# Optimization experiments

Hardware: AMD Instinct MI355X
Metric: run time of the kernel (lower is better)

## Reference

```python
import jax, jax.numpy as jnp
import numpy as np
import math

N_HEADS = 16
D_EMB = 1024
D_HEAD = D_EMB // N_HEADS


def setup_inputs() -> dict:
    key = jax.random.key(0)
    ks = jax.random.split(key, 5)
    scale_in = 1.0 / math.sqrt(D_EMB)
    x = jax.random.normal(ks[0], (2, 2048, D_EMB), dtype=jnp.float32)
    w_in = jax.random.uniform(ks[1], (3 * D_EMB, D_EMB), dtype=jnp.float32, minval=-scale_in, maxval=scale_in)
    b_in = jax.random.uniform(ks[2], (3 * D_EMB,), dtype=jnp.float32, minval=-scale_in, maxval=scale_in)
    w_out = jax.random.uniform(ks[3], (D_EMB, D_EMB), dtype=jnp.float32, minval=-scale_in, maxval=scale_in)
    b_out = jax.random.uniform(ks[4], (D_EMB,), dtype=jnp.float32, minval=-scale_in, maxval=scale_in)
    return {"x": x, "w_in": w_in, "b_in": b_in, "w_out": w_out, "b_out": b_out, "apply_mask": 1}


def reference(x, w_in, b_in, w_out, b_out, apply_mask):
    B, S, D = x.shape
    # fused QKV projection: torch Linear uses y = x @ W^T + b
    qkv = jnp.einsum('bsd,ed->bse', x, w_in) + b_in  # [B,S,3D]
    q, k, v = jnp.split(qkv, 3, axis=-1)
    # [B,H,S,Dh]
    q = q.reshape(B, S, N_HEADS, D_HEAD).transpose(0, 2, 1, 3)
    k = k.reshape(B, S, N_HEADS, D_HEAD).transpose(0, 2, 1, 3)
    v = v.reshape(B, S, N_HEADS, D_HEAD).transpose(0, 2, 1, 3)
    w = jnp.einsum('bhqd,bhkd->bhqk', q, k)  # [B,H,S,S]
    if apply_mask:
        causal = jnp.triu(jnp.ones((S, S), dtype=bool), k=1)
        w = jnp.where(causal, -jnp.inf, w)
    w = w / jnp.sqrt(jnp.float32(D_HEAD)).astype(w.dtype)
    w = jax.nn.softmax(w, axis=-1)
    score = jnp.einsum('bhqk,bhkd->bhqd', w, v)  # [B,H,S,Dh]
    score = score.transpose(0, 2, 1, 3).reshape(B, S, D)
    return jnp.einsum('bsd,ed->bse', score, w_out) + b_out
```

## Files before the change

### kernel.cpp

```cpp
#include <hip/hip_runtime.h>
#include <stdint.h>

#define DEMB 1024
#define NHEAD 16
#define DHEAD 64
#define SEQ 2048
#define MROWS 4096

typedef __bf16 bf16x8 __attribute__((ext_vector_type(8)));
typedef float f32x4 __attribute__((ext_vector_type(4)));
typedef unsigned short u16;

#define LOG2E 1.44269504088896340736f

__device__ __forceinline__ u16 f2b(float f) {
  return __builtin_bit_cast(u16, (__bf16)f);
}
__device__ __forceinline__ uint32_t pk2(float a, float b) {
  return (uint32_t)f2b(a) | ((uint32_t)f2b(b) << 16);
}

__device__ __forceinline__ f32x4 mfma16(bf16x8 a, bf16x8 b, f32x4 c) {
  return __builtin_amdgcn_mfma_f32_16x16x32_bf16(a, b, c, 0, 0, 0);
}

__device__ __forceinline__ void gload_lds16(const void* g, void* l) {
  __builtin_amdgcn_global_load_lds(
      (__attribute__((address_space(1))) unsigned int*)(g),
      (__attribute__((address_space(3))) unsigned int*)(l), 16, 0, 0);
}

__global__ void cvt3_f32_bf16(const float* __restrict__ a, int na,
                              const float* __restrict__ b, int nb,
                              const float* __restrict__ c, int nc,
                              u16* __restrict__ da, u16* __restrict__ db,
                              u16* __restrict__ dc) {
  const int total = (na + nb + nc) >> 2;
  const int stride = gridDim.x * blockDim.x;
  for (int t = blockIdx.x * blockDim.x + threadIdx.x; t < total; t += stride) {
    int i = t << 2;
    const float* s;
    u16* d;
    if (i < na) {
      s = a + i; d = da + i;
    } else if (i < na + nb) {
      s = b + (i - na); d = db + (i - na);
    } else {
      s = c + (i - na - nb); d = dc + (i - na - nb);
    }
    float4 f = *(const float4*)s;
    ushort4 o;
    o.x = f2b(f.x); o.y = f2b(f.y); o.z = f2b(f.z); o.w = f2b(f.w);
    *(ushort4*)d = o;
  }
}

template <int EPI>
__global__ __launch_bounds__(256, 4) void gemm_nt(
    const u16* __restrict__ A, const u16* __restrict__ Bw,
    const float* __restrict__ bias, int K, int N,
    u16* __restrict__ q_out, u16* __restrict__ k_out, u16* __restrict__ v_out,
    float* __restrict__ f_out) {
  __shared__ __align__(16) u16 As[128 * 64];
  __shared__ __align__(16) u16 Bs[128 * 64];
  const int tid = threadIdx.x;
  const int w = tid >> 6;
  const int lane = tid & 63;
  const int wm = w >> 1, wn = w & 1;
  const int m0 = blockIdx.y * 128, n0 = blockIdx.x * 128;
  const int l16 = lane & 15, lg = lane >> 4;
  const int st_row = lane >> 3, st_slot = lane & 7;

  f32x4 acc[4][4] = {};

  for (int k0 = 0; k0 < K; k0 += 64) {
#pragma unroll
    for (int i = 0; i < 4; ++i) {
      const int chunk = (w << 2) | i;
      const int row = (chunk << 3) | st_row;
      const int scol = (st_slot ^ (row & 7)) << 3;
      gload_lds16(A + (size_t)(m0 + row) * K + k0 + scol, (char*)As + (chunk << 10));
      gload_lds16(Bw + (size_t)(n0 + row) * K + k0 + scol, (char*)Bs + (chunk << 10));
    }
    __syncthreads();
#pragma unroll
    for (int ks = 0; ks < 2; ++ks) {
      bf16x8 af[4], bfr[4];
#pragma unroll
      for (int mi = 0; mi < 4; ++mi) {
        const int row = wm * 64 + mi * 16 + l16;
        const int cb = ((ks << 6) | (lg << 4)) ^ ((row & 7) << 4);
        af[mi] = *(const bf16x8*)((const char*)As + row * 128 + cb);
      }
#pragma unroll
      for (int ni = 0; ni < 4; ++ni) {
        const int row = wn * 64 + ni * 16 + l16;
        const int cb = ((ks << 6) | (lg << 4)) ^ ((row & 7) << 4);
        bfr[ni] = *(const bf16x8*)((const char*)Bs + row * 128 + cb);
      }
#pragma unroll
      for (int mi = 0; mi < 4; ++mi)
#pragma unroll
        for (int ni = 0; ni < 4; ++ni)
          acc[mi][ni] = mfma16(af[mi], bfr[ni], acc[mi][ni]);
    }
    __syncthreads();
  }

#pragma unroll
  for (int ni = 0; ni < 4; ++ni) {
    const int n = n0 + wn * 64 + ni * 16 + l16;
    const float bv = bias[n];
    if (EPI == 0) {
      const int part = n >> 10;
      const int hh = (n >> 6) & 15;
      const int dh = n & 63;
      if (part == 2) {
#pragma unroll
        for (int mi = 0; mi < 4; ++mi) {
          const int mbase = m0 + wm * 64 + mi * 16 + (lg << 2);
          const int bq = mbase >> 11, s0 = mbase & 2047;
          ushort4 o;
          o.x = f2b(acc[mi][ni][0] + bv);
          o.y = f2b(acc[mi][ni][1] + bv);
          o.z = f2b(acc[mi][ni][2] + bv);
          o.w = f2b(acc[mi][ni][3] + bv);
          *(ushort4*)(v_out + ((size_t)(((bq << 4) | hh) * 64 + dh)) * SEQ + s0) = o;
        }
      } else {
        const float scl = (part == 0) ? (0.125f * LOG2E) : 1.0f;
        u16* dst = (part == 0) ? q_out : k_out;
#pragma unroll
        for (int mi = 0; mi < 4; ++mi) {
#pragma unroll
          for (int i = 0; i < 4; ++i) {
            const int m = m0 + wm * 64 + mi * 16 + (lg << 2) + i;
            const int bq = m >> 11, s = m & 2047;
            dst[((size_t)((bq << 4) | hh) * SEQ + s) * DHEAD + dh] = f2b((acc[mi][ni][i] + bv) * scl);
          }
        }
      }
    } else {
#pragma unroll
      for (int mi = 0; mi < 4; ++mi)
#pragma unroll
        for (int i = 0; i < 4; ++i) {
          const int m = m0 + wm * 64 + mi * 16 + (lg << 2) + i;
          f_out[(size_t)m * N + n] = acc[mi][ni][i] + bv;
        }
    }
  }
}

__device__ __forceinline__ int swz4(int r) { return (r ^ (r >> 3)) & 15; }

__device__ __forceinline__ void stage_k(const u16* __restrict__ Kb, size_t base,
                                        int jt, u16* Ks, int w, int lane) {
#pragma unroll
  for (int i = 0; i < 4; ++i) {
    const int g = (w << 2) | i;
    const int row = (g << 2) | (lane >> 4);
    const int shat = (lane & 15) ^ swz4(row);
    const int kv = (row << 1) | (shat >> 3);
    const int del = (shat & 7) << 3;
    gload_lds16(Kb + base + (size_t)(jt * 128 + kv) * DHEAD + del,
                (char*)Ks + (g << 10));
  }
}

__device__ __forceinline__ void stage_v(const u16* __restrict__ VTg, size_t base,
                                        int jt, u16* Vs, int w, int lane) {
#pragma unroll
  for (int i = 0; i < 4; ++i) {
    const int g = (w << 2) | i;
    const int row = (g << 2) | (lane >> 4);
    const int shat = (lane & 15) ^ swz4(row);
    gload_lds16(VTg + base + (size_t)row * SEQ + jt * 128 + (shat << 3),
                (char*)Vs + (g << 10));
  }
}

__global__ __launch_bounds__(256, 2) void attn_fwd(
    const u16* __restrict__ Qb, const u16* __restrict__ Kb,
    const u16* __restrict__ VTg, u16* __restrict__ Ob,
    const int* __restrict__ amask) {
  __shared__ __align__(16) u16 Ks[2][64 * 128];
  __shared__ __align__(16) u16 Vt[2][64 * 128];
  __shared__ __align__(16) uint32_t Ps[4][1024];
  const int tid = threadIdx.x;
  const int w = tid >> 6, lane = tid & 63;
  const int l16 = lane & 15, lg = lane >> 4;

  const int id = blockIdx.x;
  const int xcd = id & 7;
  const int r = id >> 3;
  const int bh = (xcd << 2) | (r & 3);
  const int p = r >> 2;
  const int qiA = 31 - p, qiB = p;

  const size_t base = (size_t)bh * (SEQ * DHEAD);
  const bool causal = (amask[0] != 0);
  const int ntA = causal ? ((qiA >> 1) + 1) : (SEQ / 128);
  const int ntB = causal ? ((qiB >> 1) + 1) : (SEQ / 128);
  const int nt = ntA + ntB;
  const int b = bh >> 4, h = bh & 15;

  int qseg0 = qiA * 64;

  bf16x8 qf[2];
  {
    const u16* qp = Qb + base + (size_t)(qseg0 + (w << 4) + l16) * DHEAD + (lg << 3);
    qf[0] = *(const bf16x8*)qp;
    qf[1] = *(const bf16x8*)(qp + 32);
  }

  float mrow = -1e30f, lrowp = 0.f;
  f32x4 oacc[4] = {};

  const int key = (l16 & 7) << 2;
  char* prow = (char*)(&Ps[w][0]) + l16 * 256;

  stage_k(Kb, base, 0, Ks[0], w, lane);
  stage_v(VTg, base, 0, Vt[0], w, lane);
  __syncthreads();

  int cur = 0;
  for (int t = 0; t < nt; ++t) {
    const int j = (t >= ntA) ? (t - ntA) : t;
    const u16* Kcur = Ks[cur];
    const u16* Vcur = Vt[cur];
    const bool pre = (t + 1 < nt);
    const int jn = (t + 1 >= ntA) ? (t + 1 - ntA) : (t + 1);
    if (pre) stage_k(Kb, base, jn, Ks[cur ^ 1], w, lane);

    f32x4 sv[8];
    __builtin_amdgcn_s_setprio(1);
#pragma unroll
    for (int nf = 0; nf < 8; ++nf) {
      const int row2 = (nf << 3) | (l16 >> 1);
      const int sz = swz4(row2);
      const int s0 = ((l16 & 1) << 3) | lg;
      bf16x8 kf0 = *(const bf16x8*)((const char*)Kcur + row2 * 256 + ((s0 ^ sz) << 4));
      bf16x8 kf1 = *(const bf16x8*)((const char*)Kcur + row2 * 256 + (((s0 | 4) ^ sz) << 4));
      f32x4 s = {};
      s = mfma16(kf0, qf[0], s);
      s = mfma16(kf1, qf[1], s);
      sv[nf] = s;
    }
    __builtin_amdgcn_s_setprio(0);

    const bool segEnd = (t == ntA - 1) || (t == nt - 1);
    if (causal && segEnd) {
      const int q = qseg0 + (w << 4) + l16;
#pragma unroll
      for (int nf = 0; nf < 8; ++nf)
#pragma unroll
        for (int i = 0; i < 4; ++i) {
          const int kv = j * 128 + (nf << 4) + (lg << 2) + i;
          if (kv > q) sv[nf][i] = -1e30f;
        }
    }

    float tmaxg;
    {
      f32x4 mt;
#pragma unroll
      for (int i = 0; i < 4; ++i) {
        const float a01 = fmaxf(sv[0][i], sv[1][i]);
        const float a23 = fmaxf(sv[2][i], sv[3][i]);
        const float a45 = fmaxf(sv[4][i], sv[5][i]);
        const float a67 = fmaxf(sv[6][i], sv[7][i]);
        mt[i] = fmaxf(fmaxf(a01, a23), fmaxf(a45, a67));
      }
      tmaxg = fmaxf(fmaxf(mt[0], mt[1]), fmaxf(mt[2], mt[3]));
      tmaxg = fmaxf(tmaxg, __shfl_xor(tmaxg, 16));
      tmaxg = fmaxf(tmaxg, __shfl_xor(tmaxg, 32));
    }

    if (__any(tmaxg > mrow + 8.0f)) {
      const float mnew = fmaxf(mrow, tmaxg);
      const float corr = __builtin_amdgcn_exp2f(mrow - mnew);
      lrowp *= corr;
#pragma unroll
      for (int df = 0; df < 4; ++df)
#pragma unroll
        for (int i = 0; i < 4; ++i) oacc[df][i] *= corr;
      mrow = mnew;
    }

#pragma unroll
    for (int nf = 0; nf < 8; ++nf) {
      const float p0 = __builtin_amdgcn_exp2f(sv[nf][0] - mrow);
      const float p1 = __builtin_amdgcn_exp2f(sv[nf][1] - mrow);
      const float p2 = __builtin_amdgcn_exp2f(sv[nf][2] - mrow);
      const float p3 = __builtin_amdgcn_exp2f(sv[nf][3] - mrow);
      lrowp += (p0 + p1) + (p2 + p3);
      uint2 pkv;
      pkv.x = pk2(p0, p1);
      pkv.y = pk2(p2, p3);
      const int word = ((nf << 3) | (lg << 1)) ^ key;
      *(uint2*)(prow + word * 4) = pkv;
    }

    if (pre) stage_v(VTg, base, jn, Vt[cur ^ 1], w, lane);

    bf16x8 pa[4];
#pragma unroll
    for (int s = 0; s < 4; ++s)
      pa[s] = *(const bf16x8*)(prow + ((((s << 4) | (lg << 2)) ^ key) << 2));

    __builtin_amdgcn_s_setprio(1);
#pragma unroll
    for (int df = 0; df < 4; ++df) {
      const int row = (df << 4) + l16;
      const int sz = swz4(row) << 4;
#pragma unroll
      for (int s = 0; s < 4; ++s) {
        bf16x8 vf = *(const bf16x8*)((const char*)Vcur + row * 256 + (((s << 6) | (lg << 4)) ^ sz));
        oacc[df] = mfma16(vf, pa[s], oacc[df]);
      }
    }
    __builtin_amdgcn_s_setprio(0);

    if (segEnd) {
      float lrow = lrowp + __shfl_xor(lrowp, 16);
      lrow += __shfl_xor(lrow, 32);
      const float inv = 1.0f / lrow;
      const int s = qseg0 + (w << 4) + l16;
      u16* orow = Ob + (size_t)(b * SEQ + s) * DEMB + h * DHEAD;
#pragma unroll
      for (int df = 0; df < 4; ++df) {
        ushort4 o;
        o.x = f2b(oacc[df][0] * inv);
        o.y = f2b(oacc[df][1] * inv);
        o.z = f2b(oacc[df][2] * inv);
        o.w = f2b(oacc[df][3] * inv);
        *(ushort4*)(orow + (df << 4) + (lg << 2)) = o;
      }
      if (t != nt - 1) {
        qseg0 = qiB * 64;
        mrow = -1e30f;
        lrowp = 0.f;
#pragma unroll
        for (int df = 0; df < 4; ++df)
#pragma unroll
          for (int i = 0; i < 4; ++i) oacc[df][i] = 0.f;
        const u16* qp = Qb + base + (size_t)(qseg0 + (w << 4) + l16) * DHEAD + (lg << 3);
        qf[0] = *(const bf16x8*)qp;
        qf[1] = *(const bf16x8*)(qp + 32);
      }
    }

    if (pre) __syncthreads();
    cur ^= 1;
  }
}

extern "C" void kernel_launch(void* const* d_in, const int* in_sizes, int n_in,
                              void* d_out, int out_size, void* d_ws, size_t ws_size,
                              hipStream_t stream) {
  const float* x = (const float*)d_in[0];
  const float* w_in = (const float*)d_in[1];
  const float* b_in = (const float*)d_in[2];
  const float* w_out = (const float*)d_in[3];
  const float* b_out = (const float*)d_in[4];
  const int* amask = (const int*)d_in[5];
  float* out = (float*)d_out;

  u16* xb = (u16*)d_ws;
  u16* wib = xb + (size_t)MROWS * DEMB;
  u16* wob = wib + (size_t)3 * DEMB * DEMB;
  u16* Qb = wob + (size_t)DEMB * DEMB;
  u16* Kb = Qb + (size_t)MROWS * DEMB;
  u16* Vtg = Kb + (size_t)MROWS * DEMB;
  u16* Ab = xb;

  cvt3_f32_bf16<<<2048, 256, 0, stream>>>(x, MROWS * DEMB, w_in, 3 * DEMB * DEMB,
                                          w_out, DEMB * DEMB, xb, wib, wob);

  gemm_nt<0><<<dim3(24, 32), 256, 0, stream>>>(xb, wib, b_in, DEMB, 3 * DEMB,
                                               Qb, Kb, Vtg, nullptr);
  attn_fwd<<<512, 256, 0, stream>>>(Qb, Kb, Vtg, Ab, amask);
  gemm_nt<1><<<dim3(8, 32), 256, 0, stream>>>(Ab, wob, b_out, DEMB, DEMB,
                                              nullptr, nullptr, nullptr, out);
}
```

Measured before the change: 102.8 us.

## Split attention into one query tile per block with 64-key tiles

The attention kernel previously paired two causal query tiles (long and short) per block with 128-key tiles. Now each block handles one 64-row query tile over 64-key tiles, with a grid of 1024 blocks ordered so heavy and light tiles interleave. LDS buffers are halved and launch bounds raised to 4 blocks per CU to increase occupancy. In exchange there are more loop iterations with more barriers per unit of work, less work per barrier, and load balance now depends on the block scheduling order.

```diff
diff --git a/kernel.cpp b/kernel.cpp
--- a/kernel.cpp
+++ b/kernel.cpp
@@ -154,62 +154,59 @@
 
 __device__ __forceinline__ int swz4(int r) { return (r ^ (r >> 3)) & 15; }
 
-__device__ __forceinline__ void stage_k(const u16* __restrict__ Kb, size_t base,
-                                        int jt, u16* Ks, int w, int lane) {
-#pragma unroll
-  for (int i = 0; i < 4; ++i) {
-    const int g = (w << 2) | i;
+__device__ __forceinline__ void stage_k64(const u16* __restrict__ Kb, size_t base,
+                                          int jt, u16* Ks, int w, int lane) {
+#pragma unroll
+  for (int i = 0; i < 2; ++i) {
+    const int g = (w << 1) | i;
     const int row = (g << 2) | (lane >> 4);
-    const int shat = (lane & 15) ^ swz4(row);
-    const int kv = (row << 1) | (shat >> 3);
-    const int del = (shat & 7) << 3;
-    gload_lds16(Kb + base + (size_t)(jt * 128 + kv) * DHEAD + del,
+    const int sh = (lane & 15) ^ swz4(row);
+    const int kv = (row << 1) | (sh >> 3);
+    const int del = (sh & 7) << 3;
+    gload_lds16(Kb + base + (size_t)(jt * 64 + kv) * DHEAD + del,
                 (char*)Ks + (g << 10));
   }
 }
 
-__device__ __forceinline__ void stage_v(const u16* __restrict__ VTg, size_t base,
-                                        int jt, u16* Vs, int w, int lane) {
-#pragma unroll
-  for (int i = 0; i < 4; ++i) {
-    const int g = (w << 2) | i;
+__device__ __forceinline__ void stage_v64(const u16* __restrict__ VTg, size_t base,
+                                          int jt, u16* Vs, int w, int lane) {
+#pragma unroll
+  for (int i = 0; i < 2; ++i) {
+    const int g = (w << 1) | i;
     const int row = (g << 2) | (lane >> 4);
-    const int shat = (lane & 15) ^ swz4(row);
-    gload_lds16(VTg + base + (size_t)row * SEQ + jt * 128 + (shat << 3),
+    const int sh = (lane & 15) ^ swz4(row);
+    const int d = (row << 1) | (sh >> 3);
+    gload_lds16(VTg + base + (size_t)d * SEQ + jt * 64 + ((sh & 7) << 3),
                 (char*)Vs + (g << 10));
   }
 }
 
-__global__ __launch_bounds__(256, 2) void attn_fwd(
+__global__ __launch_bounds__(256, 4) void attn_fwd(
     const u16* __restrict__ Qb, const u16* __restrict__ Kb,
     const u16* __restrict__ VTg, u16* __restrict__ Ob,
     const int* __restrict__ amask) {
-  __shared__ __align__(16) u16 Ks[2][64 * 128];
-  __shared__ __align__(16) u16 Vt[2][64 * 128];
-  __shared__ __align__(16) uint32_t Ps[4][1024];
+  __shared__ __align__(16) u16 Ks[2][32 * 128];
+  __shared__ __align__(16) u16 Vt[2][32 * 128];
+  __shared__ __align__(16) uint32_t Ps[4][512];
   const int tid = threadIdx.x;
   const int w = tid >> 6, lane = tid & 63;
   const int l16 = lane & 15, lg = lane >> 4;
 
   const int id = blockIdx.x;
-  const int xcd = id & 7;
-  const int r = id >> 3;
-  const int bh = (xcd << 2) | (r & 3);
-  const int p = r >> 2;
-  const int qiA = 31 - p, qiB = p;
+  const int k5 = id >> 5;
+  const int jj = k5 & 7, qq = k5 >> 3;
+  const int qi = (qq == 0) ? 31 - jj : (qq == 1) ? jj : (qq == 2) ? 23 - jj : 8 + jj;
+  const int bh = ((id & 7) << 2) | ((id >> 3) & 3);
 
   const size_t base = (size_t)bh * (SEQ * DHEAD);
   const bool causal = (amask[0] != 0);
-  const int ntA = causal ? ((qiA >> 1) + 1) : (SEQ / 128);
-  const int ntB = causal ? ((qiB >> 1) + 1) : (SEQ / 128);
-  const int nt = ntA + ntB;
+  const int nt = causal ? (qi + 1) : (SEQ / 64);
   const int b = bh >> 4, h = bh & 15;
-
-  int qseg0 = qiA * 64;
+  const int qrow = qi * 64 + (w << 4) + l16;
 
   bf16x8 qf[2];
   {
-    const u16* qp = Qb + base + (size_t)(qseg0 + (w << 4) + l16) * DHEAD + (lg << 3);
+    const u16* qp = Qb + base + (size_t)qrow * DHEAD + (lg << 3);
     qf[0] = *(const bf16x8*)qp;
     qf[1] = *(const bf16x8*)(qp + 32);
   }
@@ -218,30 +215,28 @@
   f32x4 oacc[4] = {};
 
   const int key = (l16 & 7) << 2;
-  char* prow = (char*)(&Ps[w][0]) + l16 * 256;
-
-  stage_k(Kb, base, 0, Ks[0], w, lane);
-  stage_v(VTg, base, 0, Vt[0], w, lane);
+  char* prow = (char*)(&Ps[w][0]) + l16 * 128;
+
+  stage_k64(Kb, base, 0, Ks[0], w, lane);
+  stage_v64(VTg, base, 0, Vt[0], w, lane);
   __syncthreads();
 
   int cur = 0;
   for (int t = 0; t < nt; ++t) {
-    const int j = (t >= ntA) ? (t - ntA) : t;
     const u16* Kcur = Ks[cur];
     const u16* Vcur = Vt[cur];
     const bool pre = (t + 1 < nt);
-    const int jn = (t + 1 >= ntA) ? (t + 1 - ntA) : (t + 1);
-    if (pre) stage_k(Kb, base, jn, Ks[cur ^ 1], w, lane);
-
-    f32x4 sv[8];
+    if (pre) stage_k64(Kb, base, t + 1, Ks[cur ^ 1], w, lane);
+
+    f32x4 sv[4];
     __builtin_amdgcn_s_setprio(1);
 #pragma unroll
-    for (int nf = 0; nf < 8; ++nf) {
-      const int row2 = (nf << 3) | (l16 >> 1);
-      const int sz = swz4(row2);
+    for (int nf = 0; nf < 4; ++nf) {
+      const int r2 = (nf << 3) | (l16 >> 1);
+      const int sz = swz4(r2);
       const int s0 = ((l16 & 1) << 3) | lg;
-      bf16x8 kf0 = *(const bf16x8*)((const char*)Kcur + row2 * 256 + ((s0 ^ sz) << 4));
-      bf16x8 kf1 = *(const bf16x8*)((const char*)Kcur + row2 * 256 + (((s0 | 4) ^ sz) << 4));
+      bf16x8 kf0 = *(const bf16x8*)((const char*)Kcur + r2 * 256 + ((s0 ^ sz) << 4));
+      bf16x8 kf1 = *(const bf16x8*)((const char*)Kcur + r2 * 256 + (((s0 | 4) ^ sz) << 4));
       f32x4 s = {};
       s = mfma16(kf0, qf[0], s);
       s = mfma16(kf1, qf[1], s);
@@ -249,15 +244,13 @@
     }
     __builtin_amdgcn_s_setprio(0);
 
-    const bool segEnd = (t == ntA - 1) || (t == nt - 1);
-    if (causal && segEnd) {
-      const int q = qseg0 + (w << 4) + l16;
-#pragma unroll
-      for (int nf = 0; nf < 8; ++nf)
+    if (causal && (t == nt - 1)) {
+#pragma unroll
+      for (int nf = 0; nf < 4; ++nf)
 #pragma unroll
         for (int i = 0; i < 4; ++i) {
-          const int kv = j * 128 + (nf << 4) + (lg << 2) + i;
-          if (kv > q) sv[nf][i] = -1e30f;
+          const int kv = t * 64 + (nf << 4) + (lg << 2) + i;
+          if (kv > qrow) sv[nf][i] = -1e30f;
         }
     }
 
@@ -265,13 +258,8 @@
     {
       f32x4 mt;
 #pragma unroll
-      for (int i = 0; i < 4; ++i) {
-        const float a01 = fmaxf(sv[0][i], sv[1][i]);
-        const float a23 = fmaxf(sv[2][i], sv[3][i]);
-        const float a45 = fmaxf(sv[4][i], sv[5][i]);
-        const float a67 = fmaxf(sv[6][i], sv[7][i]);
-        mt[i] = fmaxf(fmaxf(a01, a23), fmaxf(a45, a67));
-      }
+      for (int i = 0; i < 4; ++i)
+        mt[i] = fmaxf(fmaxf(sv[0][i], sv[1][i]), fmaxf(sv[2][i], sv[3][i]));
       tmaxg = fmaxf(fmaxf(mt[0], mt[1]), fmaxf(mt[2], mt[3]));
       tmaxg = fmaxf(tmaxg, __shfl_xor(tmaxg, 16));
       tmaxg = fmaxf(tmaxg, __shfl_xor(tmaxg, 32));
@@ -289,7 +277,7 @@
     }
 
 #pragma unroll
-    for (int nf = 0; nf < 8; ++nf) {
+    for (int nf = 0; nf < 4; ++nf) {
       const float p0 = __builtin_amdgcn_exp2f(sv[nf][0] - mrow);
       const float p1 = __builtin_amdgcn_exp2f(sv[nf][1] - mrow);
       const float p2 = __builtin_amdgcn_exp2f(sv[nf][2] - mrow);
@@ -302,57 +290,45 @@
       *(uint2*)(prow + word * 4) = pkv;
     }
 
-    if (pre) stage_v(VTg, base, jn, Vt[cur ^ 1], w, lane);
-
-    bf16x8 pa[4];
-#pragma unroll
-    for (int s = 0; s < 4; ++s)
-      pa[s] = *(const bf16x8*)(prow + ((((s << 4) | (lg << 2)) ^ key) << 2));
+    if (pre) stage_v64(VTg, base, t + 1, Vt[cur ^ 1], w, lane);
+
+    bf16x8 pa[2];
+    pa[0] = *(const bf16x8*)(prow + ((((lg << 2)) ^ key) << 2));
+    pa[1] = *(const bf16x8*)(prow + (((16 | (lg << 2)) ^ key) << 2));
 
     __builtin_amdgcn_s_setprio(1);
 #pragma unroll
     for (int df = 0; df < 4; ++df) {
-      const int row = (df << 4) + l16;
-      const int sz = swz4(row) << 4;
-#pragma unroll
-      for (int s = 0; s < 4; ++s) {
-        bf16x8 vf = *(const bf16x8*)((const char*)Vcur + row * 256 + (((s << 6) | (lg << 4)) ^ sz));
+      const int r2 = (df << 3) | (l16 >> 1);
+      const int sz = swz4(r2);
+      const int pb = (l16 & 1) << 3;
+#pragma unroll
+      for (int s = 0; s < 2; ++s) {
+        bf16x8 vf = *(const bf16x8*)((const char*)Vcur + r2 * 256 +
+                                     (((pb | (s << 2) | lg) ^ sz) << 4));
         oacc[df] = mfma16(vf, pa[s], oacc[df]);
       }
     }
     __builtin_amdgcn_s_setprio(0);
 
-    if (segEnd) {
-      float lrow = lrowp + __shfl_xor(lrowp, 16);
-      lrow += __shfl_xor(lrow, 32);
-      const float inv = 1.0f / lrow;
-      const int s = qseg0 + (w << 4) + l16;
-      u16* orow = Ob + (size_t)(b * SEQ + s) * DEMB + h * DHEAD;
-#pragma unroll
-      for (int df = 0; df < 4; ++df) {
-        ushort4 o;
-        o.x = f2b(oacc[df][0] * inv);
-        o.y = f2b(oacc[df][1] * inv);
-        o.z = f2b(oacc[df][2] * inv);
-        o.w = f2b(oacc[df][3] * inv);
-        *(ushort4*)(orow + (df << 4) + (lg << 2)) = o;
-      }
-      if (t != nt - 1) {
-        qseg0 = qiB * 64;
-        mrow = -1e30f;
-        lrowp = 0.f;
-#pragma unroll
-        for (int df = 0; df < 4; ++df)
-#pragma unroll
-          for (int i = 0; i < 4; ++i) oacc[df][i] = 0.f;
-        const u16* qp = Qb + base + (size_t)(qseg0 + (w << 4) + l16) * DHEAD + (lg << 3);
-        qf[0] = *(const bf16x8*)qp;
-        qf[1] = *(const bf16x8*)(qp + 32);
-      }
-    }
-
     if (pre) __syncthreads();
     cur ^= 1;
+  }
+
+  {
+    float lrow = lrowp + __shfl_xor(lrowp, 16);
+    lrow += __shfl_xor(lrow, 32);
+    const float inv = 1.0f / lrow;
+    u16* orow = Ob + (size_t)(b * SEQ + qrow) * DEMB + h * DHEAD;
+#pragma unroll
+    for (int df = 0; df < 4; ++df) {
+      ushort4 o;
+      o.x = f2b(oacc[df][0] * inv);
+      o.y = f2b(oacc[df][1] * inv);
+      o.z = f2b(oacc[df][2] * inv);
+      o.w = f2b(oacc[df][3] * inv);
+      *(ushort4*)(orow + (df << 4) + (lg << 2)) = o;
+    }
   }
 }
 
@@ -380,7 +356,7 @@
 
   gemm_nt<0><<<dim3(24, 32), 256, 0, stream>>>(xb, wib, b_in, DEMB, 3 * DEMB,
                                                Qb, Kb, Vtg, nullptr);
-  attn_fwd<<<512, 256, 0, stream>>>(Qb, Kb, Vtg, Ab, amask);
+  attn_fwd<<<1024, 256, 0, stream>>>(Qb, Kb, Vtg, Ab, amask);
   gemm_nt<1><<<dim3(8, 32), 256, 0, stream>>>(Ab, wob, b_out, DEMB, DEMB,
                                               nullptr, nullptr, nullptr, out);
 }
```

Result: slower. 107.7 us (+4.8%).
